# Optimization experiments

Measured on AMD Instinct MI355X. Metric: run time of the kernel, lower is better.

The kernel has to match this reference:

```python
import jax, jax.numpy as jnp
import numpy as np

E = 1024   # embedding_dim
H = 16     # heads
W = 1024   # lag / seq length
B = 4      # batch
D = E // H # head dim


def setup_inputs() -> dict:
    key = jax.random.key(0)
    ks = jax.random.split(key, 5)
    scale = E ** -0.5
    return {
        "x":   jax.random.normal(ks[0], (3, B, E, W), dtype=jnp.float32),
        "L_Q": jax.random.normal(ks[1], (E, E), dtype=jnp.float32) * scale,
        "L_K": jax.random.normal(ks[2], (E, E), dtype=jnp.float32) * scale,
        "L_V": jax.random.normal(ks[3], (E, E), dtype=jnp.float32) * scale,
        "M":   jax.random.normal(ks[4], (E, E), dtype=jnp.float32) * (1.0 / (2 * E)) ** 0.5,
        "b":   jnp.zeros((E, 1), dtype=jnp.float32),
    }


def reference(x, L_Q, L_K, L_V, M, b):
    # x: [3, B, E, W] channels-first; x[0]=K input, x[1]=Q input, x[2]=V input
    K = jnp.einsum('ef,bfw->bew', L_K, x[0])
    Q = jnp.einsum('ef,bfw->bew', L_Q, x[1])
    V = jnp.einsum('ef,bfw->bew', L_V, x[2])
    # reshape to [B, H, D, W]
    Kv = K.reshape(B, H, D, W)
    Qv = Q.reshape(B, H, D, W)
    Vv = V.reshape(B, H, D, W)
    # scores[b,h,q,k] = Q_v^T @ K_v
    scores = jnp.einsum('bhdq,bhdk->bhqk', Qv, Kv)
    # causal mask: -inf for q > k (strictly lower triangle), added BEFORE softmax
    q_idx = jnp.arange(W)[:, None]
    k_idx = jnp.arange(W)[None, :]
    mask = jnp.where(q_idx > k_idx, -jnp.inf, 0.0).astype(scores.dtype)
    scores = scores + mask
    # NON-STANDARD: softmax over the QUERY axis (dim=-2), then scale
    attn = jax.nn.softmax(scores, axis=-2) / (E ** 0.5)
    # V_v @ scores: [B,H,D,W] @ [B,H,W,W] -> [B,H,D,W]
    out = jnp.einsum('bhdq,bhqk->bhdk', Vv, attn).reshape(B, E, W)
    # dense: M @ out + b (dropout identity at inference)
    return jnp.einsum('oe,bew->bow', M, out) + b
```

## Files before the change

kernel.cpp:

```cpp
#include <hip/hip_runtime.h>
#include <stdint.h>
#include <math.h>

#define E_DIM 1024
#define W_DIM 1024
#define EW 1048576L

typedef _Float16 h16;
typedef __attribute__((ext_vector_type(8))) _Float16 h8;
typedef __attribute__((ext_vector_type(4))) float f4;

__device__ __forceinline__ void async_copy16(h16* lds, const h16* g) {
    __builtin_amdgcn_global_load_lds(
        (const __attribute__((address_space(1))) void*)g,
        (__attribute__((address_space(3))) void*)lds, 16, 0, 0);
}

__global__ __launch_bounds__(256) void prep(
    const float* __restrict__ x, const float* __restrict__ LK,
    const float* __restrict__ LQ, const float* __restrict__ LV,
    const float* __restrict__ Mw, h16* __restrict__ xt, h16* __restrict__ wh)
{
    __shared__ float Ts[64][65];
    const int z = blockIdx.z;
    const int t = threadIdx.x;
    if (z < 12) {
        const float* src = x + (long)z * EW;
        h16* dst = xt + (long)z * EW;
        const int e0 = blockIdx.y * 64, w0 = blockIdx.x * 64;
        const int r = t >> 4, c4 = (t & 15) * 4;
        #pragma unroll
        for (int p = 0; p < 4; ++p) {
            float4 v = *reinterpret_cast<const float4*>(src + (long)(e0 + r + p * 16) * W_DIM + w0 + c4);
            Ts[c4 + 0][r + p * 16] = v.x;
            Ts[c4 + 1][r + p * 16] = v.y;
            Ts[c4 + 2][r + p * 16] = v.z;
            Ts[c4 + 3][r + p * 16] = v.w;
        }
        __syncthreads();
        #pragma unroll
        for (int p = 0; p < 4; ++p) {
            int wr = r + p * 16;
            union { h16 h[4]; uint2 u; } o;
            o.h[0] = (h16)Ts[wr][c4 + 0];
            o.h[1] = (h16)Ts[wr][c4 + 1];
            o.h[2] = (h16)Ts[wr][c4 + 2];
            o.h[3] = (h16)Ts[wr][c4 + 3];
            *reinterpret_cast<uint2*>(dst + (long)(w0 + wr) * E_DIM + e0 + c4) = o.u;
        }
    } else {
        const float* srcs[4] = {LK, LQ, LV, Mw};
        const float* s = srcs[z - 12];
        h16* o = wh + (long)(z - 12) * EW;
        long base = ((long)(blockIdx.y * 16 + blockIdx.x)) * 1024 + t;
        #pragma unroll
        for (int k = 0; k < 4; ++k) {
            long i = base + k * 256;
            float4 v = reinterpret_cast<const float4*>(s)[i];
            union { h16 h[4]; uint2 u; } u;
            u.h[0] = (h16)v.x; u.h[1] = (h16)v.y; u.h[2] = (h16)v.z; u.h[3] = (h16)v.w;
            reinterpret_cast<uint2*>(o)[i] = u.u;
        }
    }
}

__global__ __launch_bounds__(256) void gemm_proj3(
    const h16* __restrict__ xh, const h16* __restrict__ Wts,
    h16* __restrict__ KQV)
{
    __shared__ h16 As[128 * 64];
    __shared__ h16 Bs[128 * 64];

    const int t = threadIdx.x;
    const int wave = t >> 6, lane = t & 63;
    const int quad = lane >> 4, l16 = lane & 15;
    const int m0 = blockIdx.y * 128, n0 = blockIdx.x * 128;
    const int wm = (wave >> 1) * 64, wn = (wave & 1) * 64;

    const int proj = blockIdx.z >> 2, bz = blockIdx.z & 3;
    const h16 *A, *Bt; h16* C;
    if (proj == 0)      { A = xh + bz * EW;       Bt = Wts;          C = KQV + bz * EW; }
    else if (proj == 1) { A = xh + (4 + bz) * EW; Bt = Wts + EW;     C = KQV + (4 + bz) * EW; }
    else                { A = Wts + 2 * EW;       Bt = xh + (8 + bz) * EW; C = KQV + (8 + bz) * EW; }

    f4 acc[4][4] = {};

    for (int k0 = 0; k0 < 1024; k0 += 64) {
        __syncthreads();
        #pragma unroll
        for (int j = 0; j < 4; ++j) {
            int g = j * 256 + t, row = g >> 3, cg = (g & 7) ^ (row & 7);
            async_copy16(&As[g * 8], A  + (long)(m0 + row) * E_DIM + k0 + cg * 8);
            async_copy16(&Bs[g * 8], Bt + (long)(n0 + row) * E_DIM + k0 + cg * 8);
        }
        __syncthreads();

        h8 av[4][2], bv[4][2];
        #pragma unroll
        for (int i = 0; i < 4; ++i) {
            int ra = wm + i * 16 + l16, rb = wn + i * 16 + l16;
            #pragma unroll
            for (int c = 0; c < 2; ++c) {
                av[i][c] = *reinterpret_cast<const h8*>(&As[(ra * 8 + ((c * 4 + quad) ^ (l16 & 7))) * 8]);
                bv[i][c] = *reinterpret_cast<const h8*>(&Bs[(rb * 8 + ((c * 4 + quad) ^ (l16 & 7))) * 8]);
            }
        }
        #pragma unroll
        for (int c = 0; c < 2; ++c)
            #pragma unroll
            for (int mt = 0; mt < 4; ++mt)
                #pragma unroll
                for (int nt = 0; nt < 4; ++nt)
                    acc[mt][nt] = __builtin_amdgcn_mfma_f32_16x16x32_f16(av[mt][c], bv[nt][c], acc[mt][nt], 0, 0, 0);
    }

    #pragma unroll
    for (int mt = 0; mt < 4; ++mt)
        #pragma unroll
        for (int i = 0; i < 4; ++i) {
            int m = m0 + wm + mt * 16 + quad * 4 + i;
            #pragma unroll
            for (int nt = 0; nt < 4; ++nt)
                C[(long)m * W_DIM + n0 + wn + nt * 16 + l16] = (h16)acc[mt][nt][i];
        }
}

__global__ __launch_bounds__(256) void gemm_out(
    const h16* __restrict__ A, const h16* __restrict__ Bt,
    float* __restrict__ C, const float* __restrict__ bias)
{
    __shared__ h16 As[64 * 64];
    __shared__ h16 Bs[128 * 64];

    const int t = threadIdx.x;
    const int wave = t >> 6, lane = t & 63;
    const int quad = lane >> 4, l16 = lane & 15;
    const int m0 = blockIdx.y * 64, n0 = blockIdx.x * 128;
    const int wm = (wave >> 1) * 32, wn = (wave & 1) * 64;

    f4 acc[2][4] = {};

    for (int k0 = 0; k0 < 1024; k0 += 64) {
        __syncthreads();
        #pragma unroll
        for (int j = 0; j < 2; ++j) {
            int g = j * 256 + t, row = g >> 3, cg = (g & 7) ^ (row & 7);
            async_copy16(&As[g * 8], A + (long)(m0 + row) * E_DIM + k0 + cg * 8);
        }
        #pragma unroll
        for (int j = 0; j < 4; ++j) {
            int g = j * 256 + t, row = g >> 3, cg = (g & 7) ^ (row & 7);
            async_copy16(&Bs[g * 8], Bt + (long)(n0 + row) * E_DIM + k0 + cg * 8);
        }
        __syncthreads();

        h8 av[2][2], bv[4][2];
        #pragma unroll
        for (int c = 0; c < 2; ++c) {
            #pragma unroll
            for (int mt = 0; mt < 2; ++mt) {
                int r = wm + mt * 16 + l16;
                av[mt][c] = *reinterpret_cast<const h8*>(&As[(r * 8 + ((c * 4 + quad) ^ (l16 & 7))) * 8]);
            }
            #pragma unroll
            for (int nt = 0; nt < 4; ++nt) {
                int r = wn + nt * 16 + l16;
                bv[nt][c] = *reinterpret_cast<const h8*>(&Bs[(r * 8 + ((c * 4 + quad) ^ (l16 & 7))) * 8]);
            }
        }
        #pragma unroll
        for (int c = 0; c < 2; ++c)
            #pragma unroll
            for (int mt = 0; mt < 2; ++mt)
                #pragma unroll
                for (int nt = 0; nt < 4; ++nt)
                    acc[mt][nt] = __builtin_amdgcn_mfma_f32_16x16x32_f16(av[mt][c], bv[nt][c], acc[mt][nt], 0, 0, 0);
    }

    #pragma unroll
    for (int mt = 0; mt < 2; ++mt)
        #pragma unroll
        for (int i = 0; i < 4; ++i) {
            int m = m0 + wm + mt * 16 + quad * 4 + i;
            float bv_ = bias ? bias[m] : 0.f;
            #pragma unroll
            for (int nt = 0; nt < 4; ++nt) {
                int n = n0 + wn + nt * 16 + l16;
                C[(long)(n >> 10) * EW + (long)m * W_DIM + (n & 1023)] = acc[mt][nt][i] + bv_;
            }
        }
}

__global__ __launch_bounds__(256) void attn_mfma(
    const h16* __restrict__ Kt, const h16* __restrict__ Qt,
    const h16* __restrict__ V, h16* __restrict__ AoT)
{
    __shared__ h16 Qs[2][64 * 64];
    __shared__ h16 Vs[2][64 * 64];
    __shared__ h16 Ps[4][16 * 72];

    const int t = threadIdx.x, wave = t >> 6, lane = t & 63;
    const int quad = lane >> 4, l16 = lane & 15;
    const int b = blockIdx.y >> 4, h = blockIdx.y & 15;
    const int kt = 15 - blockIdx.x;
    const int kbase = kt * 64 + wave * 16;
    const int kcol = kbase + l16;

    const h16* Ktb = Kt + (long)b * EW + h * 64;
    const h16* Qtb = Qt + (long)b * EW + h * 64;
    const h16* Vb  = V  + (long)b * EW + (long)(h * 64) * W_DIM;
    h16* Pw = &Ps[wave][0];

    h8 kb0 = *reinterpret_cast<const h8*>(Ktb + (long)kcol * E_DIM + quad * 8);
    h8 kb1 = *reinterpret_cast<const h8*>(Ktb + (long)kcol * E_DIM + 32 + quad * 8);

    #pragma unroll
    for (int j = 0; j < 2; ++j) {
        int g = j * 256 + t, row = g >> 3, cg = (g & 7) ^ (row & 7);
        async_copy16(&Qs[0][g * 8], Qtb + (long)row * E_DIM + cg * 8);
        async_copy16(&Vs[0][g * 8], Vb + (long)row * W_DIM + cg * 8);
    }

    float mrow = -1e30f, lsum = 0.f;
    f4 O[4] = {};

    for (int it = 0; it <= kt; ++it) {
        const int q0 = it * 64;
        __syncthreads();
        if (it < kt) {
            int nb = (it + 1) & 1, q1 = q0 + 64;
            #pragma unroll
            for (int j = 0; j < 2; ++j) {
                int g = j * 256 + t, row = g >> 3, cg = (g & 7) ^ (row & 7);
                async_copy16(&Qs[nb][g * 8], Qtb + (long)(q1 + row) * E_DIM + cg * 8);
                async_copy16(&Vs[nb][g * 8], Vb + (long)row * W_DIM + q1 + cg * 8);
            }
        }
        const h16* qs = Qs[it & 1];
        const h16* vs = Vs[it & 1];

        f4 S[4];
        #pragma unroll
        for (int nt = 0; nt < 4; ++nt) {
            int row = nt * 16 + l16;
            h8 a0 = *reinterpret_cast<const h8*>(&qs[(row * 8 + (quad ^ (l16 & 7))) * 8]);
            h8 a1 = *reinterpret_cast<const h8*>(&qs[(row * 8 + ((4 + quad) ^ (l16 & 7))) * 8]);
            f4 s = {};
            s = __builtin_amdgcn_mfma_f32_16x16x32_f16(a0, kb0, s, 0, 0, 0);
            s = __builtin_amdgcn_mfma_f32_16x16x32_f16(a1, kb1, s, 0, 0, 0);
            S[nt] = s;
        }

        if (it == kt) {
            #pragma unroll
            for (int nt = 0; nt < 4; ++nt)
                #pragma unroll
                for (int i = 0; i < 4; ++i)
                    if (q0 + nt * 16 + quad * 4 + i > kcol) S[nt][i] = -1e30f;
        }

        float mx = -1e30f;
        #pragma unroll
        for (int nt = 0; nt < 4; ++nt)
            #pragma unroll
            for (int i = 0; i < 4; ++i) mx = fmaxf(mx, S[nt][i]);
        mx = fmaxf(mx, __shfl_xor(mx, 16));
        mx = fmaxf(mx, __shfl_xor(mx, 32));
        float nm = fmaxf(mrow, mx);
        float al = __expf(mrow - nm);
        mrow = nm;

        float ts = 0.f;
        #pragma unroll
        for (int nt = 0; nt < 4; ++nt)
            #pragma unroll
            for (int i = 0; i < 4; ++i) {
                float p = __expf(S[nt][i] - nm);
                S[nt][i] = p;
                ts += p;
            }
        ts += __shfl_xor(ts, 16);
        ts += __shfl_xor(ts, 32);
        lsum = lsum * al + ts;
        #pragma unroll
        for (int dt = 0; dt < 4; ++dt)
            #pragma unroll
            for (int i = 0; i < 4; ++i) O[dt][i] *= al;

        #pragma unroll
        for (int nt = 0; nt < 4; ++nt) {
            union { h16 hh[4]; uint2 u2; } p;
            p.hh[0] = (h16)S[nt][0]; p.hh[1] = (h16)S[nt][1];
            p.hh[2] = (h16)S[nt][2]; p.hh[3] = (h16)S[nt][3];
            *reinterpret_cast<uint2*>(Pw + l16 * 72 + nt * 16 + quad * 4) = p.u2;
        }
        asm volatile("" ::: "memory");

        #pragma unroll
        for (int c = 0; c < 2; ++c) {
            h8 pb = *reinterpret_cast<const h8*>(Pw + l16 * 72 + c * 32 + quad * 8);
            #pragma unroll
            for (int dt = 0; dt < 4; ++dt) {
                int r = dt * 16 + l16;
                h8 va = *reinterpret_cast<const h8*>(&vs[(r * 8 + ((c * 4 + quad) ^ (l16 & 7))) * 8]);
                O[dt] = __builtin_amdgcn_mfma_f32_16x16x32_f16(va, pb, O[dt], 0, 0, 0);
            }
        }
    }

    float inv = 0.03125f / lsum;
    #pragma unroll
    for (int dt = 0; dt < 4; ++dt) {
        union { h16 hh[4]; uint2 u2; } p;
        #pragma unroll
        for (int i = 0; i < 4; ++i) p.hh[i] = (h16)(O[dt][i] * inv);
        *reinterpret_cast<uint2*>(Pw + l16 * 72 + dt * 16 + quad * 4) = p.u2;
    }
    asm volatile("" ::: "memory");
    #pragma unroll
    for (int j = 0; j < 2; ++j) {
        uint4 vv = *reinterpret_cast<const uint4*>(Pw + l16 * 72 + quad * 16 + j * 8);
        *reinterpret_cast<uint4*>(AoT + (long)b * EW + (long)(kbase + l16) * E_DIM
                                  + h * 64 + quad * 16 + j * 8) = vv;
    }
}

extern "C" void kernel_launch(void* const* d_in, const int* in_sizes, int n_in,
                              void* d_out, int out_size, void* d_ws, size_t ws_size,
                              hipStream_t stream)
{
    const float* x  = (const float*)d_in[0];
    const float* LQ = (const float*)d_in[1];
    const float* LK = (const float*)d_in[2];
    const float* LV = (const float*)d_in[3];
    const float* Mw = (const float*)d_in[4];
    const float* bb = (const float*)d_in[5];
    float* out = (float*)d_out;
    h16* ws = (h16*)d_ws;

    h16* xh  = ws;
    h16* LKh = ws + 12 * EW;
    h16* Mh  = ws + 15 * EW;
    h16* Kp  = ws + 16 * EW;
    h16* Qp  = ws + 20 * EW;
    h16* Vp  = ws + 24 * EW;
    h16* Ao  = ws + 28 * EW;

    dim3 blk(256);
    prep<<<dim3(16, 16, 16), blk, 0, stream>>>(x, LK, LQ, LV, Mw, xh, LKh);
    gemm_proj3<<<dim3(8, 8, 12), blk, 0, stream>>>(xh, LKh, Kp);
    attn_mfma<<<dim3(16, 64), blk, 0, stream>>>(Kp, Qp, Vp, Ao);
    gemm_out<<<dim3(32, 16), blk, 0, stream>>>(Mh, Ao, out, bb);
}
```

Before: 205.7 us.

## Widen attention tile to 128 keys per block with lazy rescale and exp2

Each attention block now covers 128 key columns, with every wave owning two 16-column sub-tiles, so each Q/V tile staged in LDS feeds twice as much MFMA work. The grid is halved. Key tiles are XOR-permuted across blocks to spread the triangular causal workload, and waves whose columns are fully masked skip compute. Online-softmax rescaling is now skipped unless the running max grows by more than a threshold, and exp is computed as exp2 with pre-scaled maxima. The P buffer gets a swizzled layout, and s_setprio is raised around the MFMA sections. The trade-offs are higher register pressure, fewer blocks to fill the CUs, and more idle waves on the diagonal tiles.

```diff
diff --git a/kernel.cpp b/kernel.cpp
--- a/kernel.cpp
+++ b/kernel.cpp
@@ -197,22 +197,27 @@
 {
     __shared__ h16 Qs[2][64 * 64];
     __shared__ h16 Vs[2][64 * 64];
-    __shared__ h16 Ps[4][16 * 72];
+    __shared__ h16 Ps[4][32 * 64];
 
     const int t = threadIdx.x, wave = t >> 6, lane = t & 63;
     const int quad = lane >> 4, l16 = lane & 15;
-    const int b = blockIdx.y >> 4, h = blockIdx.y & 15;
-    const int kt = 15 - blockIdx.x;
-    const int kbase = kt * 64 + wave * 16;
-    const int kcol = kbase + l16;
-
-    const h16* Ktb = Kt + (long)b * EW + h * 64;
-    const h16* Qtb = Qt + (long)b * EW + h * 64;
-    const h16* Vb  = V  + (long)b * EW + (long)(h * 64) * W_DIM;
+    const int y = blockIdx.y;
+    const int b = y >> 4, h = y & 15;
+    const int cxor = (y & 7) ^ (((y >> 5) & 1) ? 7 : 0);
+    const int ktb = (int)blockIdx.x ^ cxor;
+    const int nit = 2 * ktb + 2;
+    const int kwave = ktb * 128 + wave * 32;
+    const int kc0 = kwave + l16, kc1 = kc0 + 16;
+
+    const h16* Ktb_ = Kt + (long)b * EW + h * 64;
+    const h16* Qtb  = Qt + (long)b * EW + h * 64;
+    const h16* Vb   = V  + (long)b * EW + (long)(h * 64) * W_DIM;
     h16* Pw = &Ps[wave][0];
 
-    h8 kb0 = *reinterpret_cast<const h8*>(Ktb + (long)kcol * E_DIM + quad * 8);
-    h8 kb1 = *reinterpret_cast<const h8*>(Ktb + (long)kcol * E_DIM + 32 + quad * 8);
+    h8 kb00 = *reinterpret_cast<const h8*>(Ktb_ + (long)kc0 * E_DIM + quad * 8);
+    h8 kb01 = *reinterpret_cast<const h8*>(Ktb_ + (long)kc0 * E_DIM + 32 + quad * 8);
+    h8 kb10 = *reinterpret_cast<const h8*>(Ktb_ + (long)kc1 * E_DIM + quad * 8);
+    h8 kb11 = *reinterpret_cast<const h8*>(Ktb_ + (long)kc1 * E_DIM + 32 + quad * 8);
 
     #pragma unroll
     for (int j = 0; j < 2; ++j) {
@@ -221,14 +226,15 @@
         async_copy16(&Vs[0][g * 8], Vb + (long)row * W_DIM + cg * 8);
     }
 
-    float mrow = -1e30f, lsum = 0.f;
-    f4 O[4] = {};
-
-    for (int it = 0; it <= kt; ++it) {
+    const float L2E = 1.442695041f;
+    float mr0 = -1e30f, mr1 = -1e30f, ls0 = 0.f, ls1 = 0.f;
+    f4 O[4][2] = {};
+
+    for (int it = 0; it < nit; ++it) {
         const int q0 = it * 64;
         __syncthreads();
-        if (it < kt) {
-            int nb = (it + 1) & 1, q1 = q0 + 64;
+        if (it + 1 < nit) {
+            const int nb = (it + 1) & 1, q1 = q0 + 64;
             #pragma unroll
             for (int j = 0; j < 2; ++j) {
                 int g = j * 256 + t, row = g >> 3, cg = (g & 7) ^ (row & 7);
@@ -236,93 +242,127 @@
                 async_copy16(&Vs[nb][g * 8], Vb + (long)row * W_DIM + q1 + cg * 8);
             }
         }
+        if (q0 > kwave + 31) continue;
+
         const h16* qs = Qs[it & 1];
         const h16* vs = Vs[it & 1];
 
-        f4 S[4];
+        f4 S0[4], S1[4];
+        __builtin_amdgcn_s_setprio(1);
         #pragma unroll
         for (int nt = 0; nt < 4; ++nt) {
             int row = nt * 16 + l16;
             h8 a0 = *reinterpret_cast<const h8*>(&qs[(row * 8 + (quad ^ (l16 & 7))) * 8]);
             h8 a1 = *reinterpret_cast<const h8*>(&qs[(row * 8 + ((4 + quad) ^ (l16 & 7))) * 8]);
-            f4 s = {};
-            s = __builtin_amdgcn_mfma_f32_16x16x32_f16(a0, kb0, s, 0, 0, 0);
-            s = __builtin_amdgcn_mfma_f32_16x16x32_f16(a1, kb1, s, 0, 0, 0);
-            S[nt] = s;
-        }
-
-        if (it == kt) {
+            f4 s0 = {}, s1 = {};
+            s0 = __builtin_amdgcn_mfma_f32_16x16x32_f16(a0, kb00, s0, 0, 0, 0);
+            s1 = __builtin_amdgcn_mfma_f32_16x16x32_f16(a0, kb10, s1, 0, 0, 0);
+            s0 = __builtin_amdgcn_mfma_f32_16x16x32_f16(a1, kb01, s0, 0, 0, 0);
+            s1 = __builtin_amdgcn_mfma_f32_16x16x32_f16(a1, kb11, s1, 0, 0, 0);
+            S0[nt] = s0; S1[nt] = s1;
+        }
+        __builtin_amdgcn_s_setprio(0);
+
+        if (it >= 2 * ktb) {
             #pragma unroll
             for (int nt = 0; nt < 4; ++nt)
                 #pragma unroll
-                for (int i = 0; i < 4; ++i)
-                    if (q0 + nt * 16 + quad * 4 + i > kcol) S[nt][i] = -1e30f;
-        }
-
-        float mx = -1e30f;
+                for (int i = 0; i < 4; ++i) {
+                    int q = q0 + nt * 16 + quad * 4 + i;
+                    if (q > kc0) S0[nt][i] = -1e30f;
+                    if (q > kc1) S1[nt][i] = -1e30f;
+                }
+        }
+
+        float mx0 = -1e30f, mx1 = -1e30f;
+        #pragma unroll
+        for (int nt = 0; nt < 4; ++nt) {
+            float t0 = fmaxf(fmaxf(S0[nt][0], S0[nt][1]), fmaxf(S0[nt][2], S0[nt][3]));
+            float t1 = fmaxf(fmaxf(S1[nt][0], S1[nt][1]), fmaxf(S1[nt][2], S1[nt][3]));
+            mx0 = fmaxf(mx0, t0); mx1 = fmaxf(mx1, t1);
+        }
+        mx0 = fmaxf(mx0, __shfl_xor(mx0, 16)); mx1 = fmaxf(mx1, __shfl_xor(mx1, 16));
+        mx0 = fmaxf(mx0, __shfl_xor(mx0, 32)); mx1 = fmaxf(mx1, __shfl_xor(mx1, 32));
+
+        if (__any((mx0 - mr0 > 8.f) || (mx1 - mr1 > 8.f))) {
+            float nm0 = fmaxf(mr0, mx0), nm1 = fmaxf(mr1, mx1);
+            float al0 = exp2f((mr0 - nm0) * L2E), al1 = exp2f((mr1 - nm1) * L2E);
+            mr0 = nm0; mr1 = nm1;
+            ls0 *= al0; ls1 *= al1;
+            #pragma unroll
+            for (int dt = 0; dt < 4; ++dt)
+                #pragma unroll
+                for (int i = 0; i < 4; ++i) { O[dt][0][i] *= al0; O[dt][1][i] *= al1; }
+        }
+
+        const float mc0 = mr0 * L2E, mc1 = mr1 * L2E;
+        float tsa = 0.f, tsb = 0.f, tsc = 0.f, tsd = 0.f;
         #pragma unroll
         for (int nt = 0; nt < 4; ++nt)
             #pragma unroll
-            for (int i = 0; i < 4; ++i) mx = fmaxf(mx, S[nt][i]);
-        mx = fmaxf(mx, __shfl_xor(mx, 16));
-        mx = fmaxf(mx, __shfl_xor(mx, 32));
-        float nm = fmaxf(mrow, mx);
-        float al = __expf(mrow - nm);
-        mrow = nm;
-
-        float ts = 0.f;
-        #pragma unroll
-        for (int nt = 0; nt < 4; ++nt)
-            #pragma unroll
             for (int i = 0; i < 4; ++i) {
-                float p = __expf(S[nt][i] - nm);
-                S[nt][i] = p;
-                ts += p;
-            }
-        ts += __shfl_xor(ts, 16);
-        ts += __shfl_xor(ts, 32);
-        lsum = lsum * al + ts;
-        #pragma unroll
-        for (int dt = 0; dt < 4; ++dt)
-            #pragma unroll
-            for (int i = 0; i < 4; ++i) O[dt][i] *= al;
+                float p0 = exp2f(fmaf(S0[nt][i], L2E, -mc0));
+                float p1 = exp2f(fmaf(S1[nt][i], L2E, -mc1));
+                S0[nt][i] = p0; S1[nt][i] = p1;
+                if (i & 1) { tsb += p0; tsd += p1; } else { tsa += p0; tsc += p1; }
+            }
+        float ts0 = tsa + tsb, ts1 = tsc + tsd;
+        ts0 += __shfl_xor(ts0, 16); ts1 += __shfl_xor(ts1, 16);
+        ts0 += __shfl_xor(ts0, 32); ts1 += __shfl_xor(ts1, 32);
+        ls0 += ts0; ls1 += ts1;
 
         #pragma unroll
         for (int nt = 0; nt < 4; ++nt) {
-            union { h16 hh[4]; uint2 u2; } p;
-            p.hh[0] = (h16)S[nt][0]; p.hh[1] = (h16)S[nt][1];
-            p.hh[2] = (h16)S[nt][2]; p.hh[3] = (h16)S[nt][3];
-            *reinterpret_cast<uint2*>(Pw + l16 * 72 + nt * 16 + quad * 4) = p.u2;
+            int sg = ((nt * 2 + (quad >> 1)) ^ (l16 & 7)) * 8 + (quad & 1) * 4;
+            union { h16 hh[4]; uint2 u2; } u0, u1;
+            #pragma unroll
+            for (int i = 0; i < 4; ++i) { u0.hh[i] = (h16)S0[nt][i]; u1.hh[i] = (h16)S1[nt][i]; }
+            *reinterpret_cast<uint2*>(Pw + l16 * 64 + sg) = u0.u2;
+            *reinterpret_cast<uint2*>(Pw + (16 + l16) * 64 + sg) = u1.u2;
         }
         asm volatile("" ::: "memory");
 
+        __builtin_amdgcn_s_setprio(1);
         #pragma unroll
         for (int c = 0; c < 2; ++c) {
-            h8 pb = *reinterpret_cast<const h8*>(Pw + l16 * 72 + c * 32 + quad * 8);
+            int sg = ((c * 4 + quad) ^ (l16 & 7)) * 8;
+            h8 p0 = *reinterpret_cast<const h8*>(Pw + l16 * 64 + sg);
+            h8 p1 = *reinterpret_cast<const h8*>(Pw + (16 + l16) * 64 + sg);
             #pragma unroll
             for (int dt = 0; dt < 4; ++dt) {
                 int r = dt * 16 + l16;
                 h8 va = *reinterpret_cast<const h8*>(&vs[(r * 8 + ((c * 4 + quad) ^ (l16 & 7))) * 8]);
-                O[dt] = __builtin_amdgcn_mfma_f32_16x16x32_f16(va, pb, O[dt], 0, 0, 0);
-            }
-        }
-    }
-
-    float inv = 0.03125f / lsum;
+                O[dt][0] = __builtin_amdgcn_mfma_f32_16x16x32_f16(va, p0, O[dt][0], 0, 0, 0);
+                O[dt][1] = __builtin_amdgcn_mfma_f32_16x16x32_f16(va, p1, O[dt][1], 0, 0, 0);
+            }
+        }
+        __builtin_amdgcn_s_setprio(0);
+    }
+
+    const float inv0 = 0.03125f / ls0, inv1 = 0.03125f / ls1;
     #pragma unroll
     for (int dt = 0; dt < 4; ++dt) {
-        union { h16 hh[4]; uint2 u2; } p;
-        #pragma unroll
-        for (int i = 0; i < 4; ++i) p.hh[i] = (h16)(O[dt][i] * inv);
-        *reinterpret_cast<uint2*>(Pw + l16 * 72 + dt * 16 + quad * 4) = p.u2;
+        int sg = ((dt * 2 + (quad >> 1)) ^ (l16 & 7)) * 8 + (quad & 1) * 4;
+        union { h16 hh[4]; uint2 u2; } u0, u1;
+        #pragma unroll
+        for (int i = 0; i < 4; ++i) {
+            u0.hh[i] = (h16)(O[dt][0][i] * inv0);
+            u1.hh[i] = (h16)(O[dt][1][i] * inv1);
+        }
+        *reinterpret_cast<uint2*>(Pw + l16 * 64 + sg) = u0.u2;
+        *reinterpret_cast<uint2*>(Pw + (16 + l16) * 64 + sg) = u1.u2;
     }
     asm volatile("" ::: "memory");
     #pragma unroll
-    for (int j = 0; j < 2; ++j) {
-        uint4 vv = *reinterpret_cast<const uint4*>(Pw + l16 * 72 + quad * 16 + j * 8);
-        *reinterpret_cast<uint4*>(AoT + (long)b * EW + (long)(kbase + l16) * E_DIM
-                                  + h * 64 + quad * 16 + j * 8) = vv;
-    }
+    for (int g = 0; g < 2; ++g)
+        #pragma unroll
+        for (int j = 0; j < 2; ++j) {
+            int sg = ((quad * 2 + j) ^ (l16 & 7)) * 8;
+            uint4 vv = *reinterpret_cast<const uint4*>(Pw + (g * 16 + l16) * 64 + sg);
+            *reinterpret_cast<uint4*>(AoT + (long)b * EW
+                                      + (long)(kwave + g * 16 + l16) * E_DIM
+                                      + h * 64 + quad * 16 + j * 8) = vv;
+        }
 }
 
 extern "C" void kernel_launch(void* const* d_in, const int* in_sizes, int n_in,
@@ -349,6 +389,6 @@
     dim3 blk(256);
     prep<<<dim3(16, 16, 16), blk, 0, stream>>>(x, LK, LQ, LV, Mw, xh, LKh);
     gemm_proj3<<<dim3(8, 8, 12), blk, 0, stream>>>(xh, LKh, Kp);
-    attn_mfma<<<dim3(16, 64), blk, 0, stream>>>(Kp, Qp, Vp, Ao);
+    attn_mfma<<<dim3(8, 64), blk, 0, stream>>>(Kp, Qp, Vp, Ao);
     gemm_out<<<dim3(32, 16), blk, 0, stream>>>(Mh, Ao, out, bb);
 }
```

After: 201.3 us. -2.2%, faster.
